# Kernel optimization log

Hardware: AMD Instinct MI355X
Metric: run time of the kernel (lower is better)

The kernel has to match this reference:

```python
import jax, jax.numpy as jnp
import numpy as np

BATCH, SEQ = 4, 2048
D_MODEL, INNER, STATE, K, FFN = 384, 768, 16, 4, 1024


def setup_inputs() -> dict:
    key = jax.random.key(0)
    ks = jax.random.split(key, 12)
    def g(k, shape, scale=0.02):
        return jax.random.normal(k, shape, jnp.float32) * scale
    return {
        "x": jax.random.normal(ks[0], (BATCH, SEQ, D_MODEL), jnp.float32),
        "rms1_w": jnp.ones((D_MODEL,), jnp.float32),
        "rms2_w": jnp.ones((D_MODEL,), jnp.float32),
        "in_proj_w": g(ks[1], (D_MODEL, 2 * INNER)),
        "conv_w": g(ks[2], (K, INNER, INNER)),
        "conv_b": jnp.zeros((INNER,), jnp.float32),
        "x_proj_w": g(ks[3], (INNER, 2 * STATE)),
        "dt_proj_w": g(ks[4], (INNER, INNER)),
        "dt_proj_b": jnp.zeros((INNER,), jnp.float32),
        "A_log": jnp.log(jax.random.uniform(ks[5], (INNER, STATE), jnp.float32, 1.0, 16.0)),
        "D_param": jnp.ones((INNER,), jnp.float32),
        "out_proj_w": g(ks[6], (INNER, D_MODEL)),
        "ln_gamma": jnp.ones((D_MODEL,), jnp.float32),
        "ln_beta": jnp.zeros((D_MODEL,), jnp.float32),
        "gate_w": g(ks[7], (D_MODEL, FFN)),
        "up_w": g(ks[8], (D_MODEL, FFN)),
        "down_w": g(ks[9], (FFN, D_MODEL)),
    }


def rms_norm(x, w, eps=1e-6):
    norm = jnp.sqrt(jnp.mean(jnp.square(x), axis=-1, keepdims=True) + eps)
    return x / norm * w


def layer_norm(x, gamma, beta, eps=1e-5):
    mu = jnp.mean(x, axis=-1, keepdims=True)
    var = jnp.mean(jnp.square(x - mu), axis=-1, keepdims=True)
    return (x - mu) / jnp.sqrt(var + eps) * gamma + beta


def selective_scan(x, delta, A_log, Bm, Cm, Dp):
    # x, delta: [B,L,Di]; Bm, Cm: [B,L,N]; A_log: [Di,N]; Dp: [Di]
    delta = jax.nn.softplus(delta)
    A = -jnp.exp(A_log)                          # [Di,N]
    A_disc = jnp.exp(delta[..., None] * A)       # [B,L,Di,N]
    B_disc = delta[..., None] * Bm[:, :, None, :]  # [B,L,Di,N]
    xs = jnp.moveaxis(x, 1, 0)       # [L,B,Di]
    As = jnp.moveaxis(A_disc, 1, 0)  # [L,B,Di,N]
    Bs = jnp.moveaxis(B_disc, 1, 0)  # [L,B,Di,N]
    Cs = jnp.moveaxis(Cm, 1, 0)      # [L,B,N]
    h0 = jnp.zeros((x.shape[0], A_log.shape[0], A_log.shape[1]), x.dtype)
    def step(h, inp):
        x_t, A_t, B_t, C_t = inp
        h = A_t * h + B_t * x_t[..., None]          # [B,Di,N]
        y_t = jnp.einsum('bdn,bn->bd', h, C_t)      # [B,Di]
        return h, y_t
    _, ys = jax.lax.scan(step, h0, (xs, As, Bs, Cs))
    y = jnp.moveaxis(ys, 0, 1)       # [B,L,Di]
    return y + Dp * x


def mamba_core(h, in_proj_w, conv_w, conv_b, x_proj_w, dt_proj_w, dt_proj_b,
               A_log, D_param, out_proj_w, ln_gamma, ln_beta):
    xz = h @ in_proj_w                             # [B,L,2*Di]
    x_inner, z = jnp.split(xz, 2, axis=-1)
    # Conv1D SAME padding (k=4 -> pad (1,2)), channels-last, kernel [W,I,O]
    x_conv = jax.lax.conv_general_dilated(
        x_inner, conv_w, window_strides=(1,), padding='SAME',
        dimension_numbers=('NWC', 'WIO', 'NWC')) + conv_b
    x_conv = jax.nn.silu(x_conv)
    Bm, Cm = jnp.split(x_conv @ x_proj_w, 2, axis=-1)  # each [B,L,N]
    delta = x_conv @ dt_proj_w + dt_proj_b            # [B,L,Di]
    y = selective_scan(x_conv, delta, A_log, Bm, Cm, D_param)
    y = y * jax.nn.silu(z)
    out = y @ out_proj_w
    return layer_norm(out, ln_gamma, ln_beta)


def reference(x, rms1_w, rms2_w, in_proj_w, conv_w, conv_b, x_proj_w,
              dt_proj_w, dt_proj_b, A_log, D_param, out_proj_w, ln_gamma,
              ln_beta, gate_w, up_w, down_w):
    residual = x
    h = rms_norm(x, rms1_w)
    h = mamba_core(h, in_proj_w, conv_w, conv_b, x_proj_w, dt_proj_w,
                   dt_proj_b, A_log, D_param, out_proj_w, ln_gamma, ln_beta)
    x = residual + h  # dropout inactive (training=False)
    residual = x
    h = rms_norm(x, rms2_w)
    hidden = jax.nn.silu(h @ gate_w) * (h @ up_w)
    x = residual + hidden @ down_w
    return x
```

## Files before the change

kernel.cpp:

```cpp
#include <hip/hip_runtime.h>
#include <hip/hip_bf16.h>


using u16 = unsigned short;
using u32 = unsigned int;
using short8 = __attribute__((ext_vector_type(8))) short;
using f32x4  = __attribute__((ext_vector_type(4))) float;

#define TTOK 8192
#define DM 384
#define DI 768
#define NST 16
#define LSEQ 2048
#define NCH 64
#define LCH 32

#define SWZ_R(row, quad) \
  ((row) * 32 + ((((quad) ^ (row) ^ ((row) >> 2)) & 3) * 8))
#define SWZ_W(tid) SWZ_R((tid) >> 2, (tid) & 3)

__device__ __forceinline__ float bf2f(u16 a) {
  u32 u = ((u32)a) << 16;
  float f; __builtin_memcpy(&f, &u, 4); return f;
}
__device__ __forceinline__ u16 f2bf(float f) {
  u32 u; __builtin_memcpy(&u, &f, 4);
  u32 r = (u + 0x7fffu + ((u >> 16) & 1u)) >> 16;
  return (u16)r;
}
__device__ __forceinline__ int probe_bf(const void* rw) {
  return (((const u32*)rw)[0] == 0x3F803F80u) ? 1 : 0;
}
__device__ __forceinline__ float ld_in(const void* p, int i, int isbf) {
  return isbf ? bf2f(((const u16*)p)[i]) : ((const float*)p)[i];
}
__device__ __forceinline__ float fexp2(float x) {
#if __has_builtin(__builtin_amdgcn_exp2f)
  return __builtin_amdgcn_exp2f(x);
#else
  return exp2f(x);
#endif
}
__device__ __forceinline__ float wave_sum(float v) {
#pragma unroll
  for (int off = 32; off > 0; off >>= 1) v += __shfl_xor(v, off, 64);
  return v;
}

__device__ __forceinline__ void gl_lds16(const u16* g, u16* l) {
  __builtin_amdgcn_global_load_lds(
      (const __attribute__((address_space(1))) u32*)g,
      (__attribute__((address_space(3))) u32*)l, 16, 0, 0);
}

#define V_CB 0
#define V_DB 768
#define V_DP 1536
#define V_R1 2304
#define V_R2 2688
#define V_GA 3072
#define V_BE 3456

__global__ __launch_bounds__(256) void k_prep(
    const void* __restrict__ x, const void* __restrict__ in_proj,
    const void* __restrict__ conv_w, const void* __restrict__ dt_w,
    const void* __restrict__ x_proj, const void* __restrict__ out_proj,
    const void* __restrict__ gate_w, const void* __restrict__ up_w,
    const void* __restrict__ down_w, const void* __restrict__ A_log,
    const void* __restrict__ conv_b, const void* __restrict__ dt_b,
    const void* __restrict__ Dp, const void* __restrict__ rms1_w,
    const void* __restrict__ rms2_w, const void* __restrict__ gamma,
    const void* __restrict__ beta,
    u16* __restrict__ W1T, u16* __restrict__ WCT, u16* __restrict__ W45T,
    u16* __restrict__ W5T, u16* __restrict__ W6T, u16* __restrict__ W7T,
    float* __restrict__ An2T, u16* __restrict__ vecs,
    u16* __restrict__ WinX, u16* __restrict__ h1pad) {
  const int isbf = probe_bf(rms1_w);
  const int bx = blockIdx.x;
  const int tid = threadIdx.x;
  __shared__ u16 lt[64 * 66];

  if (bx < 1236) {
    const void* src; size_t soff = 0; u16* dst; int R, C, tpr, lo;
    if (bx < 144)       { src = in_proj;  dst = W1T;  R = 384;  C = 1536; tpr = 24; lo = bx; }
    else if (bx < 720)  { int tp = (bx - 144) / 144; lo = (bx - 144) % 144;
                          src = conv_w; soff = (size_t)tp * 589824;
                          dst = WCT + (size_t)tp * 589824; R = 768; C = 768; tpr = 12; }
    else if (bx < 864)  { src = dt_w;     dst = W45T; R = 768;  C = 768;  tpr = 12; lo = bx - 720; }
    else if (bx < 876)  { src = x_proj;   dst = W45T + (size_t)768 * 768;
                          R = 768; C = 32; tpr = 1; lo = bx - 864; }
    else if (bx < 948)  { src = out_proj; dst = W5T;  R = 768;  C = 384;  tpr = 6;  lo = bx - 876; }
    else if (bx < 1044) { src = gate_w;   dst = W6T;  R = 384;  C = 1024; tpr = 16; lo = bx - 948; }
    else if (bx < 1140) { src = up_w;     dst = W6T + (size_t)1024 * 384;
                          R = 384; C = 1024; tpr = 16; lo = bx - 1044; }
    else                { src = down_w;   dst = W7T;  R = 1024; C = 384;  tpr = 6;  lo = bx - 1140; }
    int tr = lo / tpr, tc = lo % tpr;
    int r0 = tr * 64, c0 = tc * 64;
#pragma unroll
    for (int i = 0; i < 16; ++i) {
      int el = i * 256 + tid, lr = el >> 6, lc = el & 63;
      if (c0 + lc < C)
        lt[lr * 66 + lc] =
            f2bf(ld_in(src, (int)(soff + (size_t)(r0 + lr) * C + c0 + lc), isbf));
    }
    __syncthreads();
#pragma unroll
    for (int i = 0; i < 16; ++i) {
      int el = i * 256 + tid, orow = el >> 6, oc = el & 63;
      if (c0 + orow < C)
        dst[(size_t)(c0 + orow) * R + r0 + oc] = lt[oc * 66 + orow];
    }
    return;
  }
  if (bx < 5332) {
    int half = tid >> 7;
    int t = (bx - 1236) * 2 + half;
    int tid2 = tid & 127;
    int lane = tid & 63, wv = tid >> 6;
    float v[3]; float q = 0.f;
#pragma unroll
    for (int j = 0; j < 3; ++j) {
      v[j] = ld_in(x, t * DM + tid2 + j * 128, isbf);
      q += v[j] * v[j];
    }
    q = wave_sum(q);
    float* rq = (float*)lt;
    if (lane == 0) rq[wv] = q;
    __syncthreads();
    float rr = rsqrtf((rq[half * 2] + rq[half * 2 + 1]) * (1.f / DM) + 1e-6f);
    int b = t >> 11, l = t & 2047;
    size_t orow = ((size_t)(b * 2051 + l + 1)) * DM;
#pragma unroll
    for (int j = 0; j < 3; ++j) {
      int i = tid2 + j * 128;
      h1pad[orow + i] = f2bf(v[j] * rr * ld_in(rms1_w, i, isbf));
    }
    return;
  }
  if (bx < 6484) {
    int lo = (bx - 5332) * 256 + tid;
    int i = lo / 768, j = lo % 768;
    WinX[lo] = f2bf(ld_in(in_proj, i * 1536 + j, isbf));
    return;
  }
  if (bx < 6532) {
    int lo = (bx - 6484) * 256 + tid;
    if (lo < 12288) {
      int d = lo >> 4, n = lo & 15;
      An2T[n * DI + d] = -__expf(ld_in(A_log, lo, isbf)) * 1.44269504f;
    }
    return;
  }
  if (bx < 6547) {
    int lo = (bx - 6532) * 256 + tid;
    if (lo < 3840) {
      const void* s; int o;
      if      (lo < 768)  { s = conv_b; o = lo; }
      else if (lo < 1536) { s = dt_b;   o = lo - 768; }
      else if (lo < 2304) { s = Dp;     o = lo - 1536; }
      else if (lo < 2688) { s = rms1_w; o = lo - 2304; }
      else if (lo < 3072) { s = rms2_w; o = lo - 2688; }
      else if (lo < 3456) { s = gamma;  o = lo - 3072; }
      else                { s = beta;   o = lo - 3456; }
      vecs[lo] = f2bf(ld_in(s, o, isbf));
    }
    return;
  }
  {
    int lo = (bx - 6547) * 256 + tid;
    if (lo < 4608) {
      int b = lo / (3 * DM), rem = lo % (3 * DM);
      int which = rem / DM, i = rem % DM;
      int row = b * 2051 + (which == 0 ? 0 : (2048 + which));
      h1pad[(size_t)row * DM + i] = 0;
    }
  }
}

__global__ __launch_bounds__(128) void k_lnrms(const float* __restrict__ outm,
                                               const void* __restrict__ xin,
                                               const void* __restrict__ rw,
                                               const u16* __restrict__ vecs,
                                               float* __restrict__ x2f,
                                               u16* __restrict__ h2) {
  const int isbf = probe_bf(rw);
  int t = blockIdx.x, tid = threadIdx.x;
  int lane = tid & 63, wid = tid >> 6;
  float v[3]; float s = 0.f, q = 0.f;
#pragma unroll
  for (int j = 0; j < 3; ++j) {
    v[j] = outm[(size_t)t * DM + tid + j * 128];
    s += v[j]; q += v[j] * v[j];
  }
  s = wave_sum(s); q = wave_sum(q);
  __shared__ float rs[2], rq[2], r2[2];
  if (lane == 0) { rs[wid] = s; rq[wid] = q; }
  __syncthreads();
  float mu = (rs[0] + rs[1]) * (1.f / DM);
  float var = (rq[0] + rq[1]) * (1.f / DM) - mu * mu;
  float rstd = rsqrtf(var + 1e-5f);
  float x2v[3]; float q2 = 0.f;
#pragma unroll
  for (int j = 0; j < 3; ++j) {
    int i = tid + j * 128;
    float ln = (v[j] - mu) * rstd * bf2f(vecs[V_GA + i]) + bf2f(vecs[V_BE + i]);
    x2v[j] = ld_in(xin, t * DM + i, isbf) + ln;
    x2f[(size_t)t * DM + i] = x2v[j];
    q2 += x2v[j] * x2v[j];
  }
  q2 = wave_sum(q2);
  if (lane == 0) r2[wid] = q2;
  __syncthreads();
  float rr = rsqrtf((r2[0] + r2[1]) * (1.f / DM) + 1e-6f);
#pragma unroll
  for (int j = 0; j < 3; ++j) {
    int i = tid + j * 128;
    h2[(size_t)t * DM + i] = f2bf(x2v[j] * rr * bf2f(vecs[V_R2 + i]));
  }
}

template <int EPI, int KDIM>
__global__ __launch_bounds__(256) void gemm_bt(
    const u16* __restrict__ A, const u16* __restrict__ BT,
    float* __restrict__ o1, float* __restrict__ o2,
    u16* __restrict__ ob1, u16* __restrict__ ob2,
    const u16* __restrict__ bias, const float* __restrict__ res,
    const void* __restrict__ fl) {
  __shared__ u16 smem[2][8192];
  const int tid = threadIdx.x;
  const int lane = tid & 63, wid = tid >> 6;
  const int wm = (wid >> 1) << 5, wn = (wid & 1) << 5;
  const int fr = lane & 15, quad = lane >> 4;
  const int m0 = blockIdx.x * 64, n0 = blockIdx.y * 64;

  f32x4 acc[2][2] = {};

  const int wrow = (wid << 4) | (lane >> 2);
  const int sq = ((lane & 3) ^ wrow ^ (wrow >> 2)) & 3;
  const u16* BTe = (EPI == 6) ? BT + (size_t)blockIdx.z * 589824 : BT;
  const u16* srcA = A + (size_t)(m0 + wrow) * KDIM + sq * 8;
  const u16* srcB = BTe + (size_t)(n0 + wrow) * KDIM + sq * 8;
  u16* lw = &smem[0][0] + (wid << 9);

  auto stage = [&](int buf, int kt) {
    u16* lb = lw + buf * 8192;
    gl_lds16(srcA + kt,      lb);
    gl_lds16(srcA + kt + 32, lb + 2048);
    gl_lds16(srcB + kt,      lb + 4096);
    gl_lds16(srcB + kt + 32, lb + 6144);
  };

  stage(0, 0);
  int cur = 0;

#pragma unroll 1
  for (int kt = 0; kt < KDIM; kt += 64) {
    __syncthreads();
    if (kt + 64 < KDIM) stage(cur ^ 1, kt + 64);
    const u16* sm = &smem[cur][0];
#pragma unroll
    for (int kh = 0; kh < 2; ++kh) {
      const int ao = kh * 2048, bo = 4096 + kh * 2048;
      short8 af[2], bfg[2];
#pragma unroll
      for (int i = 0; i < 2; ++i)
        af[i] = *(const short8*)&sm[ao + SWZ_R(wm + i * 16 + fr, quad)];
#pragma unroll
      for (int i = 0; i < 2; ++i)
        bfg[i] = *(const short8*)&sm[bo + SWZ_R(wn + i * 16 + fr, quad)];
#pragma unroll
      for (int mt = 0; mt < 2; ++mt)
#pragma unroll
        for (int nt = 0; nt < 2; ++nt)
          acc[mt][nt] = __builtin_amdgcn_mfma_f32_16x16x32_bf16(
              af[mt], bfg[nt], acc[mt][nt], 0, 0, 0);
    }
    cur ^= 1;
  }

  int isbf = 0;
  if (EPI == 5) isbf = probe_bf(fl);

#pragma unroll
  for (int mt = 0; mt < 2; ++mt) {
#pragma unroll
    for (int nt = 0; nt < 2; ++nt) {
#pragma unroll
      for (int r = 0; r < 4; ++r) {
        int t = m0 + wm + mt * 16 + quad * 4 + r;
        int n = n0 + wn + nt * 16 + fr;
        float v = acc[mt][nt][r];
        if (EPI == 2) {
          if (n < DI) {
            float xx = v + bf2f(bias[n]);
            float sp = (xx > 20.f) ? xx : log1pf(__expf(xx));
            ob1[(size_t)t * DI + n] = f2bf(sp);
          } else if (n < DI + 32) {
            o2[(size_t)t * 32 + (n - DI)] = v;
          }
        } else if (EPI == 3) {
          o1[(size_t)t * DM + n] = v;
        } else if (EPI == 5) {
          float val = v + res[(size_t)t * DM + n];
          if (isbf) ob1[(size_t)t * DM + n] = f2bf(val);
          else      o1[(size_t)t * DM + n] = val;
        } else if (EPI == 6) {
          ob1[(size_t)n * 1536 + blockIdx.z * 384 + t] = f2bf(v);
        }
      }
    }
  }
}

__global__ __launch_bounds__(256) void gemm_xz(
    const u16* __restrict__ A, const u16* __restrict__ WC,
    const u16* __restrict__ WZ, u16* __restrict__ xconv,
    u16* __restrict__ zbuf, const u16* __restrict__ bias) {
  __shared__ u16 smem[2][8192];
  const int tid = threadIdx.x;
  const int lane = tid & 63, wid = tid >> 6;
  const int wm = (wid >> 1) << 5, wn = (wid & 1) << 5;
  const int fr = lane & 15, quad = lane >> 4;
  const int yb = blockIdx.y;
  const bool isz = yb >= 12;
  const int kd = isz ? 384 : 1536;
  const u16* BT = isz ? WZ : WC;
  const int kldb = isz ? 384 : 1536;
  const int n0 = (isz ? yb - 12 : yb) * 64;
  const int m0 = blockIdx.x * 64;

  f32x4 acc[2][2] = {};

  const int wrow = (wid << 4) | (lane >> 2);
  const int sq = ((lane & 3) ^ wrow ^ (wrow >> 2)) & 3;
  const u16* srcB = BT + (size_t)(n0 + wrow) * kldb + sq * 8;
  const int b = m0 >> 11, l0 = m0 & 2047;
  const u16* srcA0 =
      A + (size_t)(b * 2051 + l0 + wrow + (isz ? 1 : 0)) * DM + sq * 8;
  u16* lw = &smem[0][0] + (wid << 9);

  int wc = 0, ic = 0;
  auto stage = [&](int buf, int kt) {
    u16* lb = lw + buf * 8192;
    const u16* sa = srcA0 + (size_t)wc * DM + ic;
    gl_lds16(sa,           lb);
    gl_lds16(sa + 32,      lb + 2048);
    gl_lds16(srcB + kt,      lb + 4096);
    gl_lds16(srcB + kt + 32, lb + 6144);
    ic += 64; if (ic == 384) { ic = 0; ++wc; }
  };

  stage(0, 0);
  int cur = 0;

#pragma unroll 1
  for (int kt = 0; kt < kd; kt += 64) {
    __syncthreads();
    if (kt + 64 < kd) stage(cur ^ 1, kt + 64);
    const u16* sm = &smem[cur][0];
#pragma unroll
    for (int kh = 0; kh < 2; ++kh) {
      const int ao = kh * 2048, bo = 4096 + kh * 2048;
      short8 af[2], bfg[2];
#pragma unroll
      for (int i = 0; i < 2; ++i)
        af[i] = *(const short8*)&sm[ao + SWZ_R(wm + i * 16 + fr, quad)];
#pragma unroll
      for (int i = 0; i < 2; ++i)
        bfg[i] = *(const short8*)&sm[bo + SWZ_R(wn + i * 16 + fr, quad)];
#pragma unroll
      for (int mt = 0; mt < 2; ++mt)
#pragma unroll
        for (int nt = 0; nt < 2; ++nt)
          acc[mt][nt] = __builtin_amdgcn_mfma_f32_16x16x32_bf16(
              af[mt], bfg[nt], acc[mt][nt], 0, 0, 0);
    }
    cur ^= 1;
  }

#pragma unroll
  for (int mt = 0; mt < 2; ++mt) {
#pragma unroll
    for (int nt = 0; nt < 2; ++nt) {
#pragma unroll
      for (int r = 0; r < 4; ++r) {
        int t = m0 + wm + mt * 16 + quad * 4 + r;
        int n = n0 + wn + nt * 16 + fr;
        float v = acc[mt][nt][r];
        if (isz) {
          zbuf[(size_t)t * DI + n] = f2bf(v);
        } else {
          float xx = v + bf2f(bias[n]);
          float sg = 1.f / (1.f + __expf(-xx));
          xconv[(size_t)t * DI + n] = f2bf(xx * sg);
        }
      }
    }
  }
}

__global__ __launch_bounds__(256) void gemm_gu(
    const u16* __restrict__ A, const u16* __restrict__ W6T,
    u16* __restrict__ hid) {
  __shared__ u16 smem[12288];
  const int tid = threadIdx.x;
  const int lane = tid & 63, wid = tid >> 6;
  const int wm = (wid >> 1) << 5, wn = (wid & 1) << 5;
  const int fr = lane & 15, quad = lane >> 4;
  const int r0 = tid >> 2, c8 = (tid & 3) << 3;
  const int m0 = blockIdx.x * 64, n0 = blockIdx.y * 64;

  f32x4 accg[2][2] = {}, accu[2][2] = {};

  const u16* gA0 = A + (size_t)(m0 + r0) * DM + c8;
  const u16* gG0 = W6T + (size_t)(n0 + r0) * DM + c8;
  const u16* gU0 = W6T + (size_t)(1024 + n0 + r0) * DM + c8;

  short8 a0, a1, g00, g10, u00, u10;
  auto stage_load = [&](int kt) {
    a0  = *(const short8*)(gA0 + kt);
    a1  = *(const short8*)(gA0 + kt + 32);
    g00 = *(const short8*)(gG0 + kt);
    g10 = *(const short8*)(gG0 + kt + 32);
    u00 = *(const short8*)(gU0 + kt);
    u10 = *(const short8*)(gU0 + kt + 32);
  };

  stage_load(0);

#pragma unroll 1
  for (int kt = 0; kt < DM; kt += 64) {
    __syncthreads();
    *(short8*)&smem[SWZ_W(tid)]          = a0;
    *(short8*)&smem[2048 + SWZ_W(tid)]   = a1;
    *(short8*)&smem[4096 + SWZ_W(tid)]   = g00;
    *(short8*)&smem[6144 + SWZ_W(tid)]   = g10;
    *(short8*)&smem[8192 + SWZ_W(tid)]   = u00;
    *(short8*)&smem[10240 + SWZ_W(tid)]  = u10;
    __syncthreads();
    if (kt + 64 < DM) stage_load(kt + 64);
#pragma unroll
    for (int kh = 0; kh < 2; ++kh) {
      const int ao = kh * 2048, go = 4096 + kh * 2048, uo = 8192 + kh * 2048;
      short8 af[2], bg[2], bu[2];
#pragma unroll
      for (int i = 0; i < 2; ++i)
        af[i] = *(const short8*)&smem[ao + SWZ_R(wm + i * 16 + fr, quad)];
#pragma unroll
      for (int i = 0; i < 2; ++i) {
        bg[i] = *(const short8*)&smem[go + SWZ_R(wn + i * 16 + fr, quad)];
        bu[i] = *(const short8*)&smem[uo + SWZ_R(wn + i * 16 + fr, quad)];
      }
#pragma unroll
      for (int mt = 0; mt < 2; ++mt)
#pragma unroll
        for (int nt = 0; nt < 2; ++nt) {
          accg[mt][nt] = __builtin_amdgcn_mfma_f32_16x16x32_bf16(
              af[mt], bg[nt], accg[mt][nt], 0, 0, 0);
          accu[mt][nt] = __builtin_amdgcn_mfma_f32_16x16x32_bf16(
              af[mt], bu[nt], accu[mt][nt], 0, 0, 0);
        }
    }
  }

#pragma unroll
  for (int mt = 0; mt < 2; ++mt) {
#pragma unroll
    for (int nt = 0; nt < 2; ++nt) {
#pragma unroll
      for (int r = 0; r < 4; ++r) {
        int t = m0 + wm + mt * 16 + quad * 4 + r;
        int n = n0 + wn + nt * 16 + fr;
        float g = accg[mt][nt][r];
        float u = accu[mt][nt][r];
        float sg = 1.f / (1.f + __expf(-g));
        hid[(size_t)t * 1024 + n] = f2bf(g * sg * u);
      }
    }
  }
}

__global__ __launch_bounds__(256) void k_scan1(
    const u16* __restrict__ deltab, const u16* __restrict__ xconv,
    const float* __restrict__ BC, const float* __restrict__ An2T,
    float* __restrict__ hlb, float* __restrict__ Pb) {
  int gid = blockIdx.x * 256 + threadIdx.x;
  int d = gid % DI, bc = gid / DI, c = bc & (NCH - 1), b = bc >> 6;
  float An[NST];
#pragma unroll
  for (int n = 0; n < NST; ++n) An[n] = An2T[n * DI + d];
  float h[NST], P[NST];
#pragma unroll
  for (int n = 0; n < NST; ++n) { h[n] = 0.f; P[n] = 1.f; }
  int row0 = b * LSEQ + c * LCH;
  float dt = bf2f(deltab[(size_t)row0 * DI + d]);
  float xv = bf2f(xconv[(size_t)row0 * DI + d]);
  float4 q[4];
  {
    const float4* q4 = (const float4*)(BC + (size_t)row0 * 32);
#pragma unroll
    for (int i = 0; i < 4; ++i) q[i] = q4[i];
  }
  for (int s = 0; s < LCH; ++s) {
    float dtc = dt, xvc = xv;
    float Bm[NST];
#pragma unroll
    for (int i = 0; i < 4; ++i) {
      Bm[4*i] = q[i].x; Bm[4*i+1] = q[i].y;
      Bm[4*i+2] = q[i].z; Bm[4*i+3] = q[i].w;
    }
    if (s + 1 < LCH) {
      int r2 = row0 + s + 1;
      dt = bf2f(deltab[(size_t)r2 * DI + d]);
      xv = bf2f(xconv[(size_t)r2 * DI + d]);
      const float4* q4 = (const float4*)(BC + (size_t)r2 * 32);
#pragma unroll
      for (int i = 0; i < 4; ++i) q[i] = q4[i];
    }
    float dxv = dtc * xvc;
#pragma unroll
    for (int n = 0; n < NST; ++n) {
      float a = fexp2(dtc * An[n]);
      h[n] = fmaf(a, h[n], dxv * Bm[n]);
      P[n] *= a;
    }
  }
  float4* ph = (float4*)(hlb + (size_t)gid * NST);
  float4* pp = (float4*)(Pb + (size_t)gid * NST);
#pragma unroll
  for (int i = 0; i < 4; ++i) {
    ph[i] = make_float4(h[4*i], h[4*i+1], h[4*i+2], h[4*i+3]);
    pp[i] = make_float4(P[4*i], P[4*i+1], P[4*i+2], P[4*i+3]);
  }
}

__global__ __launch_bounds__(256) void k_scan2(const float* __restrict__ hlb,
                                               const float* __restrict__ Pb,
                                               float* __restrict__ hin) {
  int gid = blockIdx.x * 256 + threadIdx.x;
  int n = gid & 15, bd = gid >> 4;
  int d = bd % DI, b = bd / DI;
  float H = 0.f;
  for (int c = 0; c < NCH; ++c) {
    size_t idx = ((size_t)((b * NCH + c) * DI + d)) * NST + n;
    hin[idx] = H;
    H = hlb[idx] + Pb[idx] * H;
  }
}

__global__ __launch_bounds__(256) void k_scan3(
    const u16* __restrict__ deltab, const u16* __restrict__ xconv,
    const float* __restrict__ BC, const float* __restrict__ An2T,
    const float* __restrict__ hinb, const u16* __restrict__ zb,
    const u16* __restrict__ vecs, u16* __restrict__ ys) {
  int gid = blockIdx.x * 256 + threadIdx.x;
  int d = gid % DI, bc = gid / DI, c = bc & (NCH - 1), b = bc >> 6;
  float An[NST];
#pragma unroll
  for (int n = 0; n < NST; ++n) An[n] = An2T[n * DI + d];
  float h[NST];
  {
    const float4* hp = (const float4*)(hinb + (size_t)gid * NST);
#pragma unroll
    for (int i = 0; i < 4; ++i) {
      float4 t = hp[i];
      h[4*i] = t.x; h[4*i+1] = t.y; h[4*i+2] = t.z; h[4*i+3] = t.w;
    }
  }
  float Dd = bf2f(vecs[V_DP + d]);
  int row0 = b * LSEQ + c * LCH;
  float dt = bf2f(deltab[(size_t)row0 * DI + d]);
  float xv = bf2f(xconv[(size_t)row0 * DI + d]);
  float zv = bf2f(zb[(size_t)row0 * DI + d]);
  float4 q[8];
  {
    const float4* q4 = (const float4*)(BC + (size_t)row0 * 32);
#pragma unroll
    for (int i = 0; i < 8; ++i) q[i] = q4[i];
  }
  for (int s = 0; s < LCH; ++s) {
    int row = row0 + s;
    float dtc = dt, xvc = xv, zvc = zv;
    float Bm[NST], Cm[NST];
#pragma unroll
    for (int i = 0; i < 4; ++i) {
      Bm[4*i] = q[i].x;   Bm[4*i+1] = q[i].y;
      Bm[4*i+2] = q[i].z; Bm[4*i+3] = q[i].w;
      Cm[4*i] = q[4+i].x;   Cm[4*i+1] = q[4+i].y;
      Cm[4*i+2] = q[4+i].z; Cm[4*i+3] = q[4+i].w;
    }
    if (s + 1 < LCH) {
      int r2 = row + 1;
      dt = bf2f(deltab[(size_t)r2 * DI + d]);
      xv = bf2f(xconv[(size_t)r2 * DI + d]);
      zv = bf2f(zb[(size_t)r2 * DI + d]);
      const float4* q4 = (const float4*)(BC + (size_t)r2 * 32);
#pragma unroll
      for (int i = 0; i < 8; ++i) q[i] = q4[i];
    }
    float dxv = dtc * xvc;
    float yp[4] = {0.f, 0.f, 0.f, 0.f};
#pragma unroll
    for (int n = 0; n < NST; ++n) {
      float a = fexp2(dtc * An[n]);
      h[n] = fmaf(a, h[n], dxv * Bm[n]);
      yp[n & 3] = fmaf(h[n], Cm[n], yp[n & 3]);
    }
    float y = (yp[0] + yp[1]) + (yp[2] + yp[3]);
    float sz = zvc / (1.f + __expf(-zvc));
    ys[(size_t)row * DI + d] = f2bf((y + Dd * xvc) * sz);
  }
}

extern "C" void kernel_launch(void* const* d_in, const int* in_sizes, int n_in,
                              void* d_out, int out_size, void* d_ws,
                              size_t ws_size, hipStream_t stream) {
  (void)in_sizes; (void)n_in; (void)out_size;
  const void* x        = d_in[0];
  const void* rms1_w   = d_in[1];
  const void* rms2_w   = d_in[2];
  const void* in_proj  = d_in[3];
  const void* conv_w   = d_in[4];
  const void* conv_b   = d_in[5];
  const void* x_proj   = d_in[6];
  const void* dt_w     = d_in[7];
  const void* dt_b     = d_in[8];
  const void* A_log    = d_in[9];
  const void* Dp       = d_in[10];
  const void* out_proj = d_in[11];
  const void* gamma    = d_in[12];
  const void* beta     = d_in[13];
  const void* gate_w   = d_in[14];
  const void* up_w     = d_in[15];
  const void* down_w   = d_in[16];

  char* ws = (char*)d_ws;
  size_t off = 0;
  auto alloc = [&](size_t bytes) -> void* {
    void* p = ws + off;
    off = (off + bytes + 255) & ~(size_t)255;
    return p;
  };
  u16*   W1T   = (u16*)alloc((size_t)1536 * 384 * 2);
  u16*   WCT   = (u16*)alloc((size_t)4 * 768 * 768 * 2);
  u16*   W45T  = (u16*)alloc((size_t)896 * 768 * 2);
  u16*   W5T   = (u16*)alloc((size_t)384 * 768 * 2);
  u16*   W6T   = (u16*)alloc((size_t)2048 * 384 * 2);
  u16*   W7T   = (u16*)alloc((size_t)384 * 1024 * 2);
  float* An2T  = (float*)alloc((size_t)16 * 768 * 4);
  u16*   vecs  = (u16*)alloc(3840 * 2);
  u16*   WinX  = (u16*)alloc((size_t)384 * 768 * 2);
  u16*   WcombT= (u16*)alloc((size_t)768 * 1536 * 2);
  u16*   h1pad = (u16*)alloc((size_t)4 * 2051 * 384 * 2);
  u16*   zbuf  = (u16*)alloc((size_t)8192 * 768 * 2);
  u16*   xconv = (u16*)alloc((size_t)8192 * 768 * 2);
  u16*   deltab= (u16*)alloc((size_t)8192 * 768 * 2);
  float* BCb   = (float*)alloc((size_t)8192 * 32 * 4);
  float* hl    = (float*)alloc((size_t)196608 * 16 * 4);
  float* Pb    = (float*)alloc((size_t)196608 * 16 * 4);
  float* hin   = (float*)alloc((size_t)196608 * 16 * 4);
  u16*   ys   = (u16*)hl;
  float* outm = Pb;
  float* x2f  = hin;
  u16*   h2   = h1pad;
  u16*   hid  = (u16*)hl;

  if (off > ws_size) return;

  k_prep<<<6565, 256, 0, stream>>>(
      x, in_proj, conv_w, dt_w, x_proj, out_proj, gate_w, up_w, down_w,
      A_log, conv_b, dt_b, Dp, rms1_w, rms2_w, gamma, beta,
      W1T, WCT, W45T, W5T, W6T, W7T, An2T, vecs, WinX, h1pad);

  gemm_bt<6, 768><<<dim3(6, 12, 4), 256, 0, stream>>>(
      WinX, WCT, nullptr, nullptr, WcombT, nullptr, nullptr, nullptr, nullptr);

  gemm_xz<<<dim3(128, 24), 256, 0, stream>>>(
      h1pad, WcombT, W1T + (size_t)768 * 384, xconv, zbuf, vecs + V_CB);

  gemm_bt<2, 768><<<dim3(128, 13), 256, 0, stream>>>(
      xconv, W45T, nullptr, BCb, deltab, nullptr, vecs + V_DB, nullptr,
      nullptr);

  k_scan1<<<768, 256, 0, stream>>>(deltab, xconv, BCb, An2T, hl, Pb);
  k_scan2<<<192, 256, 0, stream>>>(hl, Pb, hin);
  k_scan3<<<768, 256, 0, stream>>>(deltab, xconv, BCb, An2T, hin, zbuf, vecs,
                                   ys);

  gemm_bt<3, 768><<<dim3(128, 6), 256, 0, stream>>>(
      ys, W5T, outm, nullptr, nullptr, nullptr, nullptr, nullptr, nullptr);
  k_lnrms<<<8192, 128, 0, stream>>>(outm, x, rms1_w, vecs, x2f, h2);

  gemm_gu<<<dim3(128, 16), 256, 0, stream>>>(h2, W6T, hid);
  gemm_bt<5, 1024><<<dim3(128, 6), 256, 0, stream>>>(
      hid, W7T, (float*)d_out, nullptr, (u16*)d_out, nullptr, nullptr, x2f,
      rms1_w);
}
```

Before: 320.6 us.

## Triple-buffer GEMM LDS staging and move gate/up GEMM to direct global-to-LDS loads

gemm_bt and gemm_xz go from two to three LDS stages, keeping two tiles in flight. They use an explicit vmcnt wait plus s_barrier in place of __syncthreads, so loads for tile k+2 overlap compute on tile k. gemm_gu swaps register-staged loads and LDS stores for direct global-to-LDS loads with double buffering, which removes one barrier per iteration. The extra LDS per block may lower occupancy, and the hand-written vmcnt counts must match the number of loads issued per stage.

```diff
diff --git a/kernel.cpp b/kernel.cpp
--- a/kernel.cpp
+++ b/kernel.cpp
@@ -226,7 +226,7 @@
     u16* __restrict__ ob1, u16* __restrict__ ob2,
     const u16* __restrict__ bias, const float* __restrict__ res,
     const void* __restrict__ fl) {
-  __shared__ u16 smem[2][8192];
+  __shared__ u16 smem[3][8192];
   const int tid = threadIdx.x;
   const int lane = tid & 63, wid = tid >> 6;
   const int wm = (wid >> 1) << 5, wn = (wid & 1) << 5;
@@ -251,12 +251,16 @@
   };
 
   stage(0, 0);
-  int cur = 0;
+  stage(1, 64);
+  int cur = 0, pfb = 2;
 
 #pragma unroll 1
   for (int kt = 0; kt < KDIM; kt += 64) {
-    __syncthreads();
-    if (kt + 64 < KDIM) stage(cur ^ 1, kt + 64);
+    if (kt + 64 < KDIM) asm volatile("s_waitcnt vmcnt(4)" ::: "memory");
+    else                asm volatile("s_waitcnt vmcnt(0)" ::: "memory");
+    __builtin_amdgcn_s_barrier();
+    __builtin_amdgcn_sched_barrier(0);
+    if (kt + 128 < KDIM) { stage(pfb, kt + 128); pfb = (pfb == 2) ? 0 : pfb + 1; }
     const u16* sm = &smem[cur][0];
 #pragma unroll
     for (int kh = 0; kh < 2; ++kh) {
@@ -275,7 +279,7 @@
           acc[mt][nt] = __builtin_amdgcn_mfma_f32_16x16x32_bf16(
               af[mt], bfg[nt], acc[mt][nt], 0, 0, 0);
     }
-    cur ^= 1;
+    cur = (cur == 2) ? 0 : cur + 1;
   }
 
   int isbf = 0;
@@ -316,7 +320,7 @@
     const u16* __restrict__ A, const u16* __restrict__ WC,
     const u16* __restrict__ WZ, u16* __restrict__ xconv,
     u16* __restrict__ zbuf, const u16* __restrict__ bias) {
-  __shared__ u16 smem[2][8192];
+  __shared__ u16 smem[3][8192];
   const int tid = threadIdx.x;
   const int lane = tid & 63, wid = tid >> 6;
   const int wm = (wid >> 1) << 5, wn = (wid & 1) << 5;
@@ -351,12 +355,16 @@
   };
 
   stage(0, 0);
-  int cur = 0;
+  stage(1, 64);
+  int cur = 0, pfb = 2;
 
 #pragma unroll 1
   for (int kt = 0; kt < kd; kt += 64) {
-    __syncthreads();
-    if (kt + 64 < kd) stage(cur ^ 1, kt + 64);
+    if (kt + 64 < kd) asm volatile("s_waitcnt vmcnt(4)" ::: "memory");
+    else              asm volatile("s_waitcnt vmcnt(0)" ::: "memory");
+    __builtin_amdgcn_s_barrier();
+    __builtin_amdgcn_sched_barrier(0);
+    if (kt + 128 < kd) { stage(pfb, kt + 128); pfb = (pfb == 2) ? 0 : pfb + 1; }
     const u16* sm = &smem[cur][0];
 #pragma unroll
     for (int kh = 0; kh < 2; ++kh) {
@@ -375,7 +383,7 @@
           acc[mt][nt] = __builtin_amdgcn_mfma_f32_16x16x32_bf16(
               af[mt], bfg[nt], acc[mt][nt], 0, 0, 0);
     }
-    cur ^= 1;
+    cur = (cur == 2) ? 0 : cur + 1;
   }
 
 #pragma unroll
@@ -402,54 +410,53 @@
 __global__ __launch_bounds__(256) void gemm_gu(
     const u16* __restrict__ A, const u16* __restrict__ W6T,
     u16* __restrict__ hid) {
-  __shared__ u16 smem[12288];
+  __shared__ u16 smem[2][12288];
   const int tid = threadIdx.x;
   const int lane = tid & 63, wid = tid >> 6;
   const int wm = (wid >> 1) << 5, wn = (wid & 1) << 5;
   const int fr = lane & 15, quad = lane >> 4;
-  const int r0 = tid >> 2, c8 = (tid & 3) << 3;
   const int m0 = blockIdx.x * 64, n0 = blockIdx.y * 64;
 
   f32x4 accg[2][2] = {}, accu[2][2] = {};
 
-  const u16* gA0 = A + (size_t)(m0 + r0) * DM + c8;
-  const u16* gG0 = W6T + (size_t)(n0 + r0) * DM + c8;
-  const u16* gU0 = W6T + (size_t)(1024 + n0 + r0) * DM + c8;
-
-  short8 a0, a1, g00, g10, u00, u10;
-  auto stage_load = [&](int kt) {
-    a0  = *(const short8*)(gA0 + kt);
-    a1  = *(const short8*)(gA0 + kt + 32);
-    g00 = *(const short8*)(gG0 + kt);
-    g10 = *(const short8*)(gG0 + kt + 32);
-    u00 = *(const short8*)(gU0 + kt);
-    u10 = *(const short8*)(gU0 + kt + 32);
+  const int wrow = (wid << 4) | (lane >> 2);
+  const int sq = ((lane & 3) ^ wrow ^ (wrow >> 2)) & 3;
+  const u16* srcA = A + (size_t)(m0 + wrow) * DM + sq * 8;
+  const u16* srcG = W6T + (size_t)(n0 + wrow) * DM + sq * 8;
+  const u16* srcU = W6T + (size_t)(1024 + n0 + wrow) * DM + sq * 8;
+  u16* lw = &smem[0][0] + (wid << 9);
+
+  auto stage = [&](int buf, int kt) {
+    u16* lb = lw + buf * 12288;
+    gl_lds16(srcA + kt,      lb);
+    gl_lds16(srcA + kt + 32, lb + 2048);
+    gl_lds16(srcG + kt,      lb + 4096);
+    gl_lds16(srcG + kt + 32, lb + 6144);
+    gl_lds16(srcU + kt,      lb + 8192);
+    gl_lds16(srcU + kt + 32, lb + 10240);
   };
 
-  stage_load(0);
+  stage(0, 0);
+  int cur = 0;
 
 #pragma unroll 1
   for (int kt = 0; kt < DM; kt += 64) {
-    __syncthreads();
-    *(short8*)&smem[SWZ_W(tid)]          = a0;
-    *(short8*)&smem[2048 + SWZ_W(tid)]   = a1;
-    *(short8*)&smem[4096 + SWZ_W(tid)]   = g00;
-    *(short8*)&smem[6144 + SWZ_W(tid)]   = g10;
-    *(short8*)&smem[8192 + SWZ_W(tid)]   = u00;
-    *(short8*)&smem[10240 + SWZ_W(tid)]  = u10;
-    __syncthreads();
-    if (kt + 64 < DM) stage_load(kt + 64);
+    asm volatile("s_waitcnt vmcnt(0)" ::: "memory");
+    __builtin_amdgcn_s_barrier();
+    __builtin_amdgcn_sched_barrier(0);
+    if (kt + 64 < DM) stage(cur ^ 1, kt + 64);
+    const u16* sm = &smem[cur][0];
 #pragma unroll
     for (int kh = 0; kh < 2; ++kh) {
       const int ao = kh * 2048, go = 4096 + kh * 2048, uo = 8192 + kh * 2048;
       short8 af[2], bg[2], bu[2];
 #pragma unroll
       for (int i = 0; i < 2; ++i)
-        af[i] = *(const short8*)&smem[ao + SWZ_R(wm + i * 16 + fr, quad)];
+        af[i] = *(const short8*)&sm[ao + SWZ_R(wm + i * 16 + fr, quad)];
 #pragma unroll
       for (int i = 0; i < 2; ++i) {
-        bg[i] = *(const short8*)&smem[go + SWZ_R(wn + i * 16 + fr, quad)];
-        bu[i] = *(const short8*)&smem[uo + SWZ_R(wn + i * 16 + fr, quad)];
+        bg[i] = *(const short8*)&sm[go + SWZ_R(wn + i * 16 + fr, quad)];
+        bu[i] = *(const short8*)&sm[uo + SWZ_R(wn + i * 16 + fr, quad)];
       }
 #pragma unroll
       for (int mt = 0; mt < 2; ++mt)
@@ -461,6 +468,7 @@
               af[mt], bu[nt], accu[mt][nt], 0, 0, 0);
         }
     }
+    cur ^= 1;
   }
 
 #pragma unroll
```

After: 327.9 us. 2.3% more time.

## Use 128-row GEMM tiles and stage scan B/C in shared memory

Applied to the files above, without the earlier changes.

Three GEMMs (xz conv-fused, delta/BC projection, gate/up) move from 64x64 to 128x64 tiles, with each wave computing a 64x32 sub-tile. This halves the grid and raises reuse of the B operand. The double-buffered LDS staging is replaced by single-buffer load/sync/compute, which may expose global load latency. The scan kernels now load the chunk's B/C values into shared memory once per block instead of per-thread global reads. The chunk-combine kernel prefetches the next chunk's values.

```diff
diff --git a/kernel.cpp b/kernel.cpp
--- a/kernel.cpp
+++ b/kernel.cpp
@@ -222,10 +222,8 @@
 template <int EPI, int KDIM>
 __global__ __launch_bounds__(256) void gemm_bt(
     const u16* __restrict__ A, const u16* __restrict__ BT,
-    float* __restrict__ o1, float* __restrict__ o2,
-    u16* __restrict__ ob1, u16* __restrict__ ob2,
-    const u16* __restrict__ bias, const float* __restrict__ res,
-    const void* __restrict__ fl) {
+    float* __restrict__ o1, u16* __restrict__ ob1,
+    const float* __restrict__ res, const void* __restrict__ fl) {
   __shared__ u16 smem[2][8192];
   const int tid = threadIdx.x;
   const int lane = tid & 63, wid = tid >> 6;
@@ -290,15 +288,7 @@
         int t = m0 + wm + mt * 16 + quad * 4 + r;
         int n = n0 + wn + nt * 16 + fr;
         float v = acc[mt][nt][r];
-        if (EPI == 2) {
-          if (n < DI) {
-            float xx = v + bf2f(bias[n]);
-            float sp = (xx > 20.f) ? xx : log1pf(__expf(xx));
-            ob1[(size_t)t * DI + n] = f2bf(sp);
-          } else if (n < DI + 32) {
-            o2[(size_t)t * 32 + (n - DI)] = v;
-          }
-        } else if (EPI == 3) {
+        if (EPI == 3) {
           o1[(size_t)t * DM + n] = v;
         } else if (EPI == 5) {
           float val = v + res[(size_t)t * DM + n];
@@ -312,14 +302,91 @@
   }
 }
 
+__global__ __launch_bounds__(256) void gemm2_128(
+    const u16* __restrict__ A, const u16* __restrict__ BT,
+    float* __restrict__ o2, u16* __restrict__ ob1,
+    const u16* __restrict__ bias) {
+  constexpr int KDIM = 768;
+  __shared__ u16 smem[12288];
+  const int tid = threadIdx.x;
+  const int lane = tid & 63, wid = tid >> 6;
+  const int wm = (wid >> 1) << 6, wn = (wid & 1) << 5;
+  const int fr = lane & 15, quad = lane >> 4;
+  const int m0 = blockIdx.x * 128, n0 = blockIdx.y * 64;
+
+  f32x4 acc[4][2] = {};
+
+  const int ra = (wid << 5) | (lane >> 2);
+  const int sqa = ((lane & 3) ^ ra ^ (ra >> 2)) & 3;
+  const int rb = (wid << 4) | (lane >> 2);
+  const int sqb = ((lane & 3) ^ rb ^ (rb >> 2)) & 3;
+  const u16* srcA = A + (size_t)(m0 + ra) * KDIM + sqa * 8;
+  const u16* srcB = BT + (size_t)(n0 + rb) * KDIM + sqb * 8;
+  u16* lA = &smem[0] + (wid << 10);
+  u16* lB = &smem[8192] + (wid << 9);
+
+  auto stage = [&](int kt) {
+    gl_lds16(srcA + kt,                           lA);
+    gl_lds16(srcA + kt + (size_t)16 * KDIM,       lA + 512);
+    gl_lds16(srcA + kt + 32,                      lA + 4096);
+    gl_lds16(srcA + kt + 32 + (size_t)16 * KDIM,  lA + 4608);
+    gl_lds16(srcB + kt,       lB);
+    gl_lds16(srcB + kt + 32,  lB + 2048);
+  };
+
+#pragma unroll 1
+  for (int kt = 0; kt < KDIM; kt += 64) {
+    __syncthreads();
+    stage(kt);
+    __syncthreads();
+#pragma unroll
+    for (int kh = 0; kh < 2; ++kh) {
+      const int ao = kh * 4096, bo = 8192 + kh * 2048;
+      short8 af[4], bfg[2];
+#pragma unroll
+      for (int i = 0; i < 4; ++i)
+        af[i] = *(const short8*)&smem[ao + SWZ_R(wm + i * 16 + fr, quad)];
+#pragma unroll
+      for (int i = 0; i < 2; ++i)
+        bfg[i] = *(const short8*)&smem[bo + SWZ_R(wn + i * 16 + fr, quad)];
+#pragma unroll
+      for (int mt = 0; mt < 4; ++mt)
+#pragma unroll
+        for (int nt = 0; nt < 2; ++nt)
+          acc[mt][nt] = __builtin_amdgcn_mfma_f32_16x16x32_bf16(
+              af[mt], bfg[nt], acc[mt][nt], 0, 0, 0);
+    }
+  }
+
+#pragma unroll
+  for (int mt = 0; mt < 4; ++mt) {
+#pragma unroll
+    for (int nt = 0; nt < 2; ++nt) {
+#pragma unroll
+      for (int r = 0; r < 4; ++r) {
+        int t = m0 + wm + mt * 16 + quad * 4 + r;
+        int n = n0 + wn + nt * 16 + fr;
+        float v = acc[mt][nt][r];
+        if (n < DI) {
+          float xx = v + bf2f(bias[n]);
+          float sp = (xx > 20.f) ? xx : log1pf(__expf(xx));
+          ob1[(size_t)t * DI + n] = f2bf(sp);
+        } else if (n < DI + 32) {
+          o2[(size_t)t * 32 + (n - DI)] = v;
+        }
+      }
+    }
+  }
+}
+
 __global__ __launch_bounds__(256) void gemm_xz(
     const u16* __restrict__ A, const u16* __restrict__ WC,
     const u16* __restrict__ WZ, u16* __restrict__ xconv,
     u16* __restrict__ zbuf, const u16* __restrict__ bias) {
-  __shared__ u16 smem[2][8192];
+  __shared__ u16 smem[12288];
   const int tid = threadIdx.x;
   const int lane = tid & 63, wid = tid >> 6;
-  const int wm = (wid >> 1) << 5, wn = (wid & 1) << 5;
+  const int wm = (wid >> 1) << 6, wn = (wid & 1) << 5;
   const int fr = lane & 15, quad = lane >> 4;
   const int yb = blockIdx.y;
   const bool isz = yb >= 12;
@@ -327,59 +394,59 @@
   const u16* BT = isz ? WZ : WC;
   const int kldb = isz ? 384 : 1536;
   const int n0 = (isz ? yb - 12 : yb) * 64;
-  const int m0 = blockIdx.x * 64;
-
-  f32x4 acc[2][2] = {};
-
-  const int wrow = (wid << 4) | (lane >> 2);
-  const int sq = ((lane & 3) ^ wrow ^ (wrow >> 2)) & 3;
-  const u16* srcB = BT + (size_t)(n0 + wrow) * kldb + sq * 8;
+  const int m0 = blockIdx.x * 128;
+
+  f32x4 acc[4][2] = {};
+
+  const int ra = (wid << 5) | (lane >> 2);
+  const int sqa = ((lane & 3) ^ ra ^ (ra >> 2)) & 3;
+  const int rb = (wid << 4) | (lane >> 2);
+  const int sqb = ((lane & 3) ^ rb ^ (rb >> 2)) & 3;
+  const u16* srcB = BT + (size_t)(n0 + rb) * kldb + sqb * 8;
   const int b = m0 >> 11, l0 = m0 & 2047;
   const u16* srcA0 =
-      A + (size_t)(b * 2051 + l0 + wrow + (isz ? 1 : 0)) * DM + sq * 8;
-  u16* lw = &smem[0][0] + (wid << 9);
+      A + (size_t)(b * 2051 + l0 + ra + (isz ? 1 : 0)) * DM + sqa * 8;
+  u16* lA = &smem[0] + (wid << 10);
+  u16* lB = &smem[8192] + (wid << 9);
 
   int wc = 0, ic = 0;
-  auto stage = [&](int buf, int kt) {
-    u16* lb = lw + buf * 8192;
+  auto stage = [&](int kt) {
     const u16* sa = srcA0 + (size_t)wc * DM + ic;
-    gl_lds16(sa,           lb);
-    gl_lds16(sa + 32,      lb + 2048);
-    gl_lds16(srcB + kt,      lb + 4096);
-    gl_lds16(srcB + kt + 32, lb + 6144);
+    gl_lds16(sa,                         lA);
+    gl_lds16(sa + (size_t)16 * DM,       lA + 512);
+    gl_lds16(sa + 32,                    lA + 4096);
+    gl_lds16(sa + 32 + (size_t)16 * DM,  lA + 4608);
+    gl_lds16(srcB + kt,       lB);
+    gl_lds16(srcB + kt + 32,  lB + 2048);
     ic += 64; if (ic == 384) { ic = 0; ++wc; }
   };
 
-  stage(0, 0);
-  int cur = 0;
-
 #pragma unroll 1
   for (int kt = 0; kt < kd; kt += 64) {
     __syncthreads();
-    if (kt + 64 < kd) stage(cur ^ 1, kt + 64);
-    const u16* sm = &smem[cur][0];
+    stage(kt);
+    __syncthreads();
 #pragma unroll
     for (int kh = 0; kh < 2; ++kh) {
-      const int ao = kh * 2048, bo = 4096 + kh * 2048;
-      short8 af[2], bfg[2];
+      const int ao = kh * 4096, bo = 8192 + kh * 2048;
+      short8 af[4], bfg[2];
+#pragma unroll
+      for (int i = 0; i < 4; ++i)
+        af[i] = *(const short8*)&smem[ao + SWZ_R(wm + i * 16 + fr, quad)];
 #pragma unroll
       for (int i = 0; i < 2; ++i)
-        af[i] = *(const short8*)&sm[ao + SWZ_R(wm + i * 16 + fr, quad)];
-#pragma unroll
-      for (int i = 0; i < 2; ++i)
-        bfg[i] = *(const short8*)&sm[bo + SWZ_R(wn + i * 16 + fr, quad)];
-#pragma unroll
-      for (int mt = 0; mt < 2; ++mt)
+        bfg[i] = *(const short8*)&smem[bo + SWZ_R(wn + i * 16 + fr, quad)];
+#pragma unroll
+      for (int mt = 0; mt < 4; ++mt)
 #pragma unroll
         for (int nt = 0; nt < 2; ++nt)
           acc[mt][nt] = __builtin_amdgcn_mfma_f32_16x16x32_bf16(
               af[mt], bfg[nt], acc[mt][nt], 0, 0, 0);
     }
-    cur ^= 1;
-  }
-
-#pragma unroll
-  for (int mt = 0; mt < 2; ++mt) {
+  }
+
+#pragma unroll
+  for (int mt = 0; mt < 4; ++mt) {
 #pragma unroll
     for (int nt = 0; nt < 2; ++nt) {
 #pragma unroll
@@ -402,49 +469,48 @@
 __global__ __launch_bounds__(256) void gemm_gu(
     const u16* __restrict__ A, const u16* __restrict__ W6T,
     u16* __restrict__ hid) {
-  __shared__ u16 smem[12288];
+  __shared__ u16 smem[16384];
   const int tid = threadIdx.x;
   const int lane = tid & 63, wid = tid >> 6;
-  const int wm = (wid >> 1) << 5, wn = (wid & 1) << 5;
+  const int wm = (wid >> 1) << 6, wn = (wid & 1) << 5;
   const int fr = lane & 15, quad = lane >> 4;
-  const int r0 = tid >> 2, c8 = (tid & 3) << 3;
-  const int m0 = blockIdx.x * 64, n0 = blockIdx.y * 64;
-
-  f32x4 accg[2][2] = {}, accu[2][2] = {};
-
-  const u16* gA0 = A + (size_t)(m0 + r0) * DM + c8;
-  const u16* gG0 = W6T + (size_t)(n0 + r0) * DM + c8;
-  const u16* gU0 = W6T + (size_t)(1024 + n0 + r0) * DM + c8;
-
-  short8 a0, a1, g00, g10, u00, u10;
-  auto stage_load = [&](int kt) {
-    a0  = *(const short8*)(gA0 + kt);
-    a1  = *(const short8*)(gA0 + kt + 32);
-    g00 = *(const short8*)(gG0 + kt);
-    g10 = *(const short8*)(gG0 + kt + 32);
-    u00 = *(const short8*)(gU0 + kt);
-    u10 = *(const short8*)(gU0 + kt + 32);
+  const int m0 = blockIdx.x * 128, n0 = blockIdx.y * 64;
+
+  f32x4 accg[4][2] = {}, accu[4][2] = {};
+
+  const int ra = (wid << 5) | (lane >> 2);
+  const int sqa = ((lane & 3) ^ ra ^ (ra >> 2)) & 3;
+  const int rb = (wid << 4) | (lane >> 2);
+  const int sqb = ((lane & 3) ^ rb ^ (rb >> 2)) & 3;
+  const u16* srcA = A + (size_t)(m0 + ra) * DM + sqa * 8;
+  const u16* srcG = W6T + (size_t)(n0 + rb) * DM + sqb * 8;
+  const u16* srcU = W6T + (size_t)(1024 + n0 + rb) * DM + sqb * 8;
+  u16* lA = &smem[0] + (wid << 10);
+  u16* lG = &smem[8192] + (wid << 9);
+  u16* lU = &smem[12288] + (wid << 9);
+
+  auto stage = [&](int kt) {
+    gl_lds16(srcA + kt,                        lA);
+    gl_lds16(srcA + kt + (size_t)16 * DM,      lA + 512);
+    gl_lds16(srcA + kt + 32,                   lA + 4096);
+    gl_lds16(srcA + kt + 32 + (size_t)16 * DM, lA + 4608);
+    gl_lds16(srcG + kt,       lG);
+    gl_lds16(srcG + kt + 32,  lG + 2048);
+    gl_lds16(srcU + kt,       lU);
+    gl_lds16(srcU + kt + 32,  lU + 2048);
   };
-
-  stage_load(0);
 
 #pragma unroll 1
   for (int kt = 0; kt < DM; kt += 64) {
     __syncthreads();
-    *(short8*)&smem[SWZ_W(tid)]          = a0;
-    *(short8*)&smem[2048 + SWZ_W(tid)]   = a1;
-    *(short8*)&smem[4096 + SWZ_W(tid)]   = g00;
-    *(short8*)&smem[6144 + SWZ_W(tid)]   = g10;
-    *(short8*)&smem[8192 + SWZ_W(tid)]   = u00;
-    *(short8*)&smem[10240 + SWZ_W(tid)]  = u10;
-    __syncthreads();
-    if (kt + 64 < DM) stage_load(kt + 64);
+    stage(kt);
+    __syncthreads();
 #pragma unroll
     for (int kh = 0; kh < 2; ++kh) {
-      const int ao = kh * 2048, go = 4096 + kh * 2048, uo = 8192 + kh * 2048;
-      short8 af[2], bg[2], bu[2];
-#pragma unroll
-      for (int i = 0; i < 2; ++i)
+      const int ao = kh * 4096, go = 8192 + kh * 2048, uo = 12288 + kh * 2048;
+      short8 af[4], bg[2], bu[2];
+#pragma unroll
+      for (int i = 0; i < 4; ++i)
         af[i] = *(const short8*)&smem[ao + SWZ_R(wm + i * 16 + fr, quad)];
 #pragma unroll
       for (int i = 0; i < 2; ++i) {
@@ -452,7 +518,7 @@
         bu[i] = *(const short8*)&smem[uo + SWZ_R(wn + i * 16 + fr, quad)];
       }
 #pragma unroll
-      for (int mt = 0; mt < 2; ++mt)
+      for (int mt = 0; mt < 4; ++mt)
 #pragma unroll
         for (int nt = 0; nt < 2; ++nt) {
           accg[mt][nt] = __builtin_amdgcn_mfma_f32_16x16x32_bf16(
@@ -464,7 +530,7 @@
   }
 
 #pragma unroll
-  for (int mt = 0; mt < 2; ++mt) {
+  for (int mt = 0; mt < 4; ++mt) {
 #pragma unroll
     for (int nt = 0; nt < 2; ++nt) {
 #pragma unroll
@@ -484,39 +550,32 @@
     const u16* __restrict__ deltab, const u16* __restrict__ xconv,
     const float* __restrict__ BC, const float* __restrict__ An2T,
     float* __restrict__ hlb, float* __restrict__ Pb) {
+  __shared__ float bcs[LCH * 32];
   int gid = blockIdx.x * 256 + threadIdx.x;
   int d = gid % DI, bc = gid / DI, c = bc & (NCH - 1), b = bc >> 6;
+  int row0 = b * LSEQ + c * LCH;
+  ((float4*)bcs)[threadIdx.x] =
+      ((const float4*)(BC + (size_t)row0 * 32))[threadIdx.x];
   float An[NST];
 #pragma unroll
   for (int n = 0; n < NST; ++n) An[n] = An2T[n * DI + d];
   float h[NST], P[NST];
 #pragma unroll
   for (int n = 0; n < NST; ++n) { h[n] = 0.f; P[n] = 1.f; }
-  int row0 = b * LSEQ + c * LCH;
   float dt = bf2f(deltab[(size_t)row0 * DI + d]);
   float xv = bf2f(xconv[(size_t)row0 * DI + d]);
-  float4 q[4];
-  {
-    const float4* q4 = (const float4*)(BC + (size_t)row0 * 32);
-#pragma unroll
-    for (int i = 0; i < 4; ++i) q[i] = q4[i];
-  }
+  __syncthreads();
   for (int s = 0; s < LCH; ++s) {
     float dtc = dt, xvc = xv;
-    float Bm[NST];
-#pragma unroll
-    for (int i = 0; i < 4; ++i) {
-      Bm[4*i] = q[i].x; Bm[4*i+1] = q[i].y;
-      Bm[4*i+2] = q[i].z; Bm[4*i+3] = q[i].w;
-    }
     if (s + 1 < LCH) {
       int r2 = row0 + s + 1;
       dt = bf2f(deltab[(size_t)r2 * DI + d]);
       xv = bf2f(xconv[(size_t)r2 * DI + d]);
-      const float4* q4 = (const float4*)(BC + (size_t)r2 * 32);
-#pragma unroll
-      for (int i = 0; i < 4; ++i) q[i] = q4[i];
-    }
+    }
+    const float4* br = (const float4*)&bcs[s * 32];
+    float4 q0 = br[0], q1 = br[1], q2 = br[2], q3 = br[3];
+    float Bm[NST] = {q0.x, q0.y, q0.z, q0.w, q1.x, q1.y, q1.z, q1.w,
+                     q2.x, q2.y, q2.z, q2.w, q3.x, q3.y, q3.z, q3.w};
     float dxv = dtc * xvc;
 #pragma unroll
     for (int n = 0; n < NST; ++n) {
@@ -540,11 +599,17 @@
   int gid = blockIdx.x * 256 + threadIdx.x;
   int n = gid & 15, bd = gid >> 4;
   int d = bd % DI, b = bd / DI;
+  size_t base = ((size_t)(b * NCH) * DI + d) * NST + n;
+  const size_t cstride = (size_t)DI * NST;
   float H = 0.f;
+  float hc = hlb[base], pc = Pb[base];
   for (int c = 0; c < NCH; ++c) {
-    size_t idx = ((size_t)((b * NCH + c) * DI + d)) * NST + n;
+    size_t idx = base + (size_t)c * cstride;
+    float hn = 0.f, pn = 0.f;
+    if (c + 1 < NCH) { hn = hlb[idx + cstride]; pn = Pb[idx + cstride]; }
     hin[idx] = H;
-    H = hlb[idx] + Pb[idx] * H;
+    H = hc + pc * H;
+    hc = hn; pc = pn;
   }
 }
 
@@ -553,8 +618,12 @@
     const float* __restrict__ BC, const float* __restrict__ An2T,
     const float* __restrict__ hinb, const u16* __restrict__ zb,
     const u16* __restrict__ vecs, u16* __restrict__ ys) {
+  __shared__ float bcs[LCH * 32];
   int gid = blockIdx.x * 256 + threadIdx.x;
   int d = gid % DI, bc = gid / DI, c = bc & (NCH - 1), b = bc >> 6;
+  int row0 = b * LSEQ + c * LCH;
+  ((float4*)bcs)[threadIdx.x] =
+      ((const float4*)(BC + (size_t)row0 * 32))[threadIdx.x];
   float An[NST];
 #pragma unroll
   for (int n = 0; n < NST; ++n) An[n] = An2T[n * DI + d];
@@ -568,36 +637,26 @@
     }
   }
   float Dd = bf2f(vecs[V_DP + d]);
-  int row0 = b * LSEQ + c * LCH;
   float dt = bf2f(deltab[(size_t)row0 * DI + d]);
   float xv = bf2f(xconv[(size_t)row0 * DI + d]);
   float zv = bf2f(zb[(size_t)row0 * DI + d]);
-  float4 q[8];
-  {
-    const float4* q4 = (const float4*)(BC + (size_t)row0 * 32);
-#pragma unroll
-    for (int i = 0; i < 8; ++i) q[i] = q4[i];
-  }
+  __syncthreads();
   for (int s = 0; s < LCH; ++s) {
     int row = row0 + s;
     float dtc = dt, xvc = xv, zvc = zv;
-    float Bm[NST], Cm[NST];
-#pragma unroll
-    for (int i = 0; i < 4; ++i) {
-      Bm[4*i] = q[i].x;   Bm[4*i+1] = q[i].y;
-      Bm[4*i+2] = q[i].z; Bm[4*i+3] = q[i].w;
-      Cm[4*i] = q[4+i].x;   Cm[4*i+1] = q[4+i].y;
-      Cm[4*i+2] = q[4+i].z; Cm[4*i+3] = q[4+i].w;
-    }
     if (s + 1 < LCH) {
       int r2 = row + 1;
       dt = bf2f(deltab[(size_t)r2 * DI + d]);
       xv = bf2f(xconv[(size_t)r2 * DI + d]);
       zv = bf2f(zb[(size_t)r2 * DI + d]);
-      const float4* q4 = (const float4*)(BC + (size_t)r2 * 32);
-#pragma unroll
-      for (int i = 0; i < 8; ++i) q[i] = q4[i];
-    }
+    }
+    const float4* br = (const float4*)&bcs[s * 32];
+    float4 q0 = br[0], q1 = br[1], q2 = br[2], q3 = br[3];
+    float4 c0 = br[4], c1 = br[5], c2 = br[6], c3 = br[7];
+    float Bm[NST] = {q0.x, q0.y, q0.z, q0.w, q1.x, q1.y, q1.z, q1.w,
+                     q2.x, q2.y, q2.z, q2.w, q3.x, q3.y, q3.z, q3.w};
+    float Cm[NST] = {c0.x, c0.y, c0.z, c0.w, c1.x, c1.y, c1.z, c1.w,
+                     c2.x, c2.y, c2.z, c2.w, c3.x, c3.y, c3.z, c3.w};
     float dxv = dtc * xvc;
     float yp[4] = {0.f, 0.f, 0.f, 0.f};
 #pragma unroll
@@ -673,14 +732,13 @@
       W1T, WCT, W45T, W5T, W6T, W7T, An2T, vecs, WinX, h1pad);
 
   gemm_bt<6, 768><<<dim3(6, 12, 4), 256, 0, stream>>>(
-      WinX, WCT, nullptr, nullptr, WcombT, nullptr, nullptr, nullptr, nullptr);
-
-  gemm_xz<<<dim3(128, 24), 256, 0, stream>>>(
+      WinX, WCT, nullptr, WcombT, nullptr, nullptr);
+
+  gemm_xz<<<dim3(64, 24), 256, 0, stream>>>(
       h1pad, WcombT, W1T + (size_t)768 * 384, xconv, zbuf, vecs + V_CB);
 
-  gemm_bt<2, 768><<<dim3(128, 13), 256, 0, stream>>>(
-      xconv, W45T, nullptr, BCb, deltab, nullptr, vecs + V_DB, nullptr,
-      nullptr);
+  gemm2_128<<<dim3(64, 13), 256, 0, stream>>>(
+      xconv, W45T, BCb, deltab, vecs + V_DB);
 
   k_scan1<<<768, 256, 0, stream>>>(deltab, xconv, BCb, An2T, hl, Pb);
   k_scan2<<<192, 256, 0, stream>>>(hl, Pb, hin);
@@ -688,11 +746,10 @@
                                    ys);
 
   gemm_bt<3, 768><<<dim3(128, 6), 256, 0, stream>>>(
-      ys, W5T, outm, nullptr, nullptr, nullptr, nullptr, nullptr, nullptr);
+      ys, W5T, outm, nullptr, nullptr, nullptr);
   k_lnrms<<<8192, 128, 0, stream>>>(outm, x, rms1_w, vecs, x2f, h2);
 
-  gemm_gu<<<dim3(128, 16), 256, 0, stream>>>(h2, W6T, hid);
+  gemm_gu<<<dim3(64, 16), 256, 0, stream>>>(h2, W6T, hid);
   gemm_bt<5, 1024><<<dim3(128, 6), 256, 0, stream>>>(
-      hid, W7T, (float*)d_out, nullptr, (u16*)d_out, nullptr, nullptr, x2f,
-      rms1_w);
-}
+      hid, W7T, (float*)d_out, (u16*)d_out, x2f, rms1_w);
+}
```

After: 313.5 us. 1.02x faster.
